# Performance work log

Hardware: AMD Instinct MI355X
Metric: run time of the kernel (lower is better)

## Reference

```python
import jax, jax.numpy as jnp
import numpy as np

ENC = 1024
DEC = 1024


def setup_inputs() -> dict:
    key = jax.random.key(0)
    k = jax.random.split(key, 8)
    s1 = 1.0 / np.sqrt(ENC)
    s2 = 1.0 / np.sqrt(DEC)
    return {
        "encoder_outputs": jax.random.normal(k[0], (32, 2048, ENC), jnp.float32),
        "decoder_output": jax.random.normal(k[1], (32, 1, DEC), jnp.float32),
        "w1": jax.random.uniform(k[2], (ENC, ENC), jnp.float32, -s1, s1),
        "b1": jax.random.uniform(k[3], (ENC,), jnp.float32, -s1, s1),
        "w2": jax.random.uniform(k[4], (DEC, ENC), jnp.float32, -s2, s2),
        "b2": jax.random.uniform(k[5], (ENC,), jnp.float32, -s2, s2),
        "v": jax.random.uniform(k[6], (ENC, 1), jnp.float32, -s1, s1),
        "bv": jax.random.uniform(k[7], (1,), jnp.float32, -s1, s1),
    }


def reference(encoder_outputs, decoder_output, w1, b1, w2, b2, v, bv):
    # [B,1,E] query projection, broadcast-added to [B,S,E] key projection
    w2_dec = jnp.einsum("bqd,de->bqe", decoder_output, w2) + b2
    w1_enc = jnp.einsum("bsd,de->bse", encoder_outputs, w1) + b1
    scores = jnp.einsum("bse,eo->bso", jnp.tanh(w1_enc + w2_dec), v) + bv  # [B,S,1]
    attn = jax.nn.softmax(scores[..., 0], axis=1)  # softmax over sequence dim
    context = jnp.einsum("bs,bse->be", attn, encoder_outputs)  # [B,E]
    return context
```

## Files before the change

kernel.cpp:

```cpp
#include <hip/hip_runtime.h>
#include <hip/hip_bf16.h>


typedef __attribute__((ext_vector_type(8))) short short8;
typedef __attribute__((ext_vector_type(4))) float f32x4;

#define M_TOTAL 65536
#define KDIM    1024

static __device__ inline unsigned int pk2h(float a, float b) {
    unsigned int ua = __builtin_bit_cast(unsigned int, a) + 0x8000u;
    unsigned int ub = __builtin_bit_cast(unsigned int, b) + 0x8000u;
    return __builtin_amdgcn_perm(ub, ua, 0x07060302u);
}

static __device__ inline void async_copy16(const void* g, void* l) {
    __builtin_amdgcn_global_load_lds(
        (const __attribute__((address_space(1))) unsigned int*)g,
        (__attribute__((address_space(3))) unsigned int*)l, 16, 0, 0);
}

__global__ void pack_w1(const float* __restrict__ w1, unsigned short* __restrict__ w1p) {
    __shared__ float tile[32][33];
    const int tx = threadIdx.x, ty = threadIdx.y;
    tile[ty][tx] = w1[(blockIdx.y * 32 + ty) * 1024 + blockIdx.x * 32 + tx];
    __syncthreads();
    const int eo = blockIdx.x * 32 + ty;
    const int dq = blockIdx.y * 32 + tx;
    const unsigned int u = __builtin_bit_cast(unsigned int, tile[tx][ty]) + 0x8000u;
    const unsigned short us = (unsigned short)(u >> 16);
    const int nt = eo >> 7, r = eo & 127;
    const int kc = dq >> 6, c = (dq >> 3) & 7, j = dq & 7;
    const int cs = c ^ (r & 7);
    w1p[(((size_t)(nt * 16 + kc)) << 13) + (r << 6) + (cs << 3) + j] = us;
}

__global__ __launch_bounds__(256) void qq_kern(const float* __restrict__ dec,
                                               const float* __restrict__ w2,
                                               const float* __restrict__ b1,
                                               const float* __restrict__ b2,
                                               float* __restrict__ qq) {
    const int b = blockIdx.y;
    const int e = blockIdx.x * 256 + threadIdx.x;
    const int d0 = blockIdx.z * 256;
    const float* db = dec + b * 1024;
    float acc = (blockIdx.z == 0) ? (b1[e] + b2[e]) : 0.f;
#pragma unroll 8
    for (int d = d0; d < d0 + 256; d++)
        acc = fmaf(db[d], w2[d * 1024 + e], acc);
    atomicAdd(&qq[b * 1024 + e], acc);
}

static __device__ inline void score_epilogue(f32x4 acc[4][4], const float* qqb,
                                             const float* vvec, float* scores,
                                             int m0, int n0, int wm, int wn,
                                             int quad, int lc) {
    const int nb = n0 + wn * 64 + lc;
    float qn[4], vn[4];
#pragma unroll
    for (int ni = 0; ni < 4; ni++) {
        qn[ni] = qqb[nb + ni * 16];
        vn[ni] = vvec[nb + ni * 16];
    }
    float red[16];
#pragma unroll
    for (int mi = 0; mi < 4; mi++) {
#pragma unroll
        for (int r = 0; r < 4; r++) {
            float ssum = 0.f;
#pragma unroll
            for (int ni = 0; ni < 4; ni++) {
                float x = acc[mi][ni][r] + qn[ni];
                float e = __expf(2.0f * x);
                float th = 1.0f - 2.0f / (e + 1.0f);
                ssum = fmaf(th, vn[ni], ssum);
            }
            float t = ssum;
            t += __shfl_xor(t, 1);
            t += __shfl_xor(t, 2);
            t += __shfl_xor(t, 4);
            t += __shfl_xor(t, 8);
            red[mi * 4 + r] = t;
        }
    }
    float myv = red[0];
#pragma unroll
    for (int i = 1; i < 16; i++)
        if (lc == i) myv = red[i];
    atomicAdd(scores + m0 + wm * 64 + (lc >> 2) * 16 + quad * 4 + (lc & 3), myv);
}

__global__ __launch_bounds__(256) void score_gemm(const float* __restrict__ enc,
                                                  const unsigned short* __restrict__ w1p,
                                                  const float* __restrict__ qq,
                                                  const float* __restrict__ vvec,
                                                  float* __restrict__ scores) {
    __shared__ __align__(16) unsigned short As[128 * 64];
    __shared__ __align__(16) unsigned short Bs[128 * 64];

    const int g = blockIdx.x;
    const int mtile = (g & 7) * 64 + (g >> 6);
    const int ntile = (g >> 3) & 7;
    const int m0 = mtile * 128;
    const int b = m0 >> 11;

    const int tid = threadIdx.x;
    const int wid = tid >> 6;
    const int lane = tid & 63;
    const int wm = wid >> 1, wn = wid & 1;
    const int quad = lane >> 4, lc = lane & 15;
    const int swz = lc & 7;
    const int fc0 = ((quad ^ swz) << 3);
    const int fc1 = (((4 + quad) ^ swz) << 3);

    const int sr0 = tid >> 3;
    const int sc = tid & 7;

    f32x4 acc[4][4];
#pragma unroll
    for (int mi = 0; mi < 4; mi++)
#pragma unroll
        for (int ni = 0; ni < 4; ni++)
            acc[mi][ni] = (f32x4){0.f, 0.f, 0.f, 0.f};

    const unsigned short* bbase = w1p + ((size_t)ntile << 17) + (wid << 11) + (lane << 3);
    unsigned short* bdst = &Bs[wid << 11];

    for (int k0 = 0; k0 < KDIM; k0 += 64) {
        __syncthreads();

        const unsigned short* bsrc = bbase + (((size_t)(k0 >> 6)) << 13);
        async_copy16(bsrc, bdst);
        async_copy16(bsrc + 512, bdst + 512);
        async_copy16(bsrc + 1024, bdst + 1024);
        async_copy16(bsrc + 1536, bdst + 1536);

        float4 fv[8];
#pragma unroll
        for (int j = 0; j < 4; j++) {
            const float* src = enc + (size_t)(m0 + sr0 + 32 * j) * 1024 + k0 + sc * 8;
            fv[2 * j]     = *reinterpret_cast<const float4*>(src);
            fv[2 * j + 1] = *reinterpret_cast<const float4*>(src + 4);
        }
#pragma unroll
        for (int j = 0; j < 4; j++) {
            const int r = sr0 + 32 * j;
            uint4 w;
            w.x = pk2h(fv[2 * j].x, fv[2 * j].y);
            w.y = pk2h(fv[2 * j].z, fv[2 * j].w);
            w.z = pk2h(fv[2 * j + 1].x, fv[2 * j + 1].y);
            w.w = pk2h(fv[2 * j + 1].z, fv[2 * j + 1].w);
            *reinterpret_cast<uint4*>(&As[(r << 6) + ((sc ^ (r & 7)) << 3)]) = w;
        }

        __syncthreads();

        short8 af[4], bf[4];
#pragma unroll
        for (int i = 0; i < 4; i++) {
            af[i] = *reinterpret_cast<const short8*>(&As[((wm * 64 + i * 16 + lc) << 6) + fc0]);
            bf[i] = *reinterpret_cast<const short8*>(&Bs[((wn * 64 + i * 16 + lc) << 6) + fc0]);
        }
#pragma unroll
        for (int mi = 0; mi < 4; mi++)
#pragma unroll
            for (int ni = 0; ni < 4; ni++)
                acc[mi][ni] = __builtin_amdgcn_mfma_f32_16x16x32_bf16(af[mi], bf[ni], acc[mi][ni], 0, 0, 0);
#pragma unroll
        for (int i = 0; i < 4; i++) {
            af[i] = *reinterpret_cast<const short8*>(&As[((wm * 64 + i * 16 + lc) << 6) + fc1]);
            bf[i] = *reinterpret_cast<const short8*>(&Bs[((wn * 64 + i * 16 + lc) << 6) + fc1]);
        }
#pragma unroll
        for (int mi = 0; mi < 4; mi++)
#pragma unroll
            for (int ni = 0; ni < 4; ni++)
                acc[mi][ni] = __builtin_amdgcn_mfma_f32_16x16x32_bf16(af[mi], bf[ni], acc[mi][ni], 0, 0, 0);
    }

    score_epilogue(acc, qq + b * 1024, vvec, scores, m0, ntile * 128, wm, wn, quad, lc);
}

__global__ __launch_bounds__(256) void softmax_kern(const float* __restrict__ scores,
                                                    float* __restrict__ attn) {
    const int b = blockIdx.x;
    const int tid = threadIdx.x;
    const int wid = tid >> 6, lane = tid & 63;
    const float* s = scores + b * 2048;
    float x[8];
    float m = -1e30f;
#pragma unroll
    for (int i = 0; i < 8; i++) {
        x[i] = s[tid + i * 256];
        m = fmaxf(m, x[i]);
    }
    for (int off = 1; off < 64; off <<= 1) m = fmaxf(m, __shfl_xor(m, off));
    __shared__ float redm[4];
    if (lane == 0) redm[wid] = m;
    __syncthreads();
    m = fmaxf(fmaxf(redm[0], redm[1]), fmaxf(redm[2], redm[3]));
    float sum = 0.f;
#pragma unroll
    for (int i = 0; i < 8; i++) {
        x[i] = __expf(x[i] - m);
        sum += x[i];
    }
    for (int off = 1; off < 64; off <<= 1) sum += __shfl_xor(sum, off);
    __shared__ float reds[4];
    if (lane == 0) reds[wid] = sum;
    __syncthreads();
    sum = reds[0] + reds[1] + reds[2] + reds[3];
    const float inv = 1.0f / sum;
#pragma unroll
    for (int i = 0; i < 8; i++) attn[b * 2048 + tid + i * 256] = x[i] * inv;
}

__global__ __launch_bounds__(256) void ctx_kern(const float* __restrict__ attn,
                                                const float* __restrict__ enc,
                                                float* __restrict__ out) {
    const int b = blockIdx.y;
    const int sc = blockIdx.x;
    const int tid = threadIdx.x;
    const float* ab = attn + b * 2048 + sc * 64;
    const float* eb = enc + ((size_t)b * 2048 + sc * 64) * 1024 + tid * 4;
    float4 acc = {0.f, 0.f, 0.f, 0.f};
#pragma unroll 16
    for (int s = 0; s < 64; s++) {
        float w = ab[s];
        float4 ev = *reinterpret_cast<const float4*>(eb + (size_t)s * 1024);
        acc.x = fmaf(w, ev.x, acc.x);
        acc.y = fmaf(w, ev.y, acc.y);
        acc.z = fmaf(w, ev.z, acc.z);
        acc.w = fmaf(w, ev.w, acc.w);
    }
    float* op = out + b * 1024 + tid * 4;
    atomicAdd(op + 0, acc.x);
    atomicAdd(op + 1, acc.y);
    atomicAdd(op + 2, acc.z);
    atomicAdd(op + 3, acc.w);
}

extern "C" void kernel_launch(void* const* d_in, const int* in_sizes, int n_in,
                              void* d_out, int out_size, void* d_ws, size_t ws_size,
                              hipStream_t stream) {
    const float* enc = (const float*)d_in[0];
    const float* dec = (const float*)d_in[1];
    const float* w1  = (const float*)d_in[2];
    const float* b1  = (const float*)d_in[3];
    const float* w2  = (const float*)d_in[4];
    const float* b2  = (const float*)d_in[5];
    const float* v   = (const float*)d_in[6];
    float* out = (float*)d_out;

    char* ws = (char*)d_ws;
    unsigned short* w1p = (unsigned short*)ws;
    float* qq     = (float*)(ws + (2u << 20));
    float* scores = (float*)(ws + (2u << 20) + (128u << 10));
    float* attn   = scores + M_TOTAL;

    hipMemsetAsync(qq, 0, (128u << 10) + M_TOTAL * sizeof(float), stream);
    hipMemsetAsync(out, 0, 32 * 1024 * sizeof(float), stream);

    pack_w1<<<dim3(32, 32), dim3(32, 32), 0, stream>>>(w1, w1p);
    qq_kern<<<dim3(4, 32, 4), 256, 0, stream>>>(dec, w2, b1, b2, qq);
    score_gemm<<<4096, 256, 0, stream>>>(enc, w1p, qq, v, scores);
    softmax_kern<<<32, 256, 0, stream>>>(scores, attn);
    ctx_kern<<<dim3(32, 32), 256, 0, stream>>>(attn, enc, out);
}
```

Measured before the change: 651.7 us.

## Double-buffer LDS tiles in score GEMM to overlap loads with MFMA

Turns the single-buffered K loop of the score GEMM into a two-stage software pipeline with ping-pong LDS buffers. The next tile's W1 async copy and encoder fp32 loads are issued before the current tile's MFMAs, and the bf16 pack into LDS happens after them, so global latency is meant to overlap compute. It also drops one barrier per iteration. LDS use doubles to 64KB per block and register pressure rises from holding the prefetched fv across compute, which can lower occupancy.

Measured after the change: 672.4 us. 1.03x slower.

```diff
diff --git a/kernel.cpp b/kernel.cpp
--- a/kernel.cpp
+++ b/kernel.cpp
@@ -7,6 +7,7 @@
 
 #define M_TOTAL 65536
 #define KDIM    1024
+#define KT_N    16
 
 static __device__ inline unsigned int pk2h(float a, float b) {
     unsigned int ua = __builtin_bit_cast(unsigned int, a) + 0x8000u;
@@ -95,8 +96,8 @@
                                                   const float* __restrict__ qq,
                                                   const float* __restrict__ vvec,
                                                   float* __restrict__ scores) {
-    __shared__ __align__(16) unsigned short As[128 * 64];
-    __shared__ __align__(16) unsigned short Bs[128 * 64];
+    __shared__ __align__(16) unsigned short As[2][128 * 64];
+    __shared__ __align__(16) unsigned short Bs[2][128 * 64];
 
     const int g = blockIdx.x;
     const int mtile = (g & 7) * 64 + (g >> 6);
@@ -124,24 +125,25 @@
             acc[mi][ni] = (f32x4){0.f, 0.f, 0.f, 0.f};
 
     const unsigned short* bbase = w1p + ((size_t)ntile << 17) + (wid << 11) + (lane << 3);
-    unsigned short* bdst = &Bs[wid << 11];
-
-    for (int k0 = 0; k0 < KDIM; k0 += 64) {
-        __syncthreads();
-
-        const unsigned short* bsrc = bbase + (((size_t)(k0 >> 6)) << 13);
+    float4 fv[8];
+
+    auto issueB = [&](int kt, int pb) {
+        const unsigned short* bsrc = bbase + ((size_t)kt << 13);
+        unsigned short* bdst = &Bs[pb][wid << 11];
         async_copy16(bsrc, bdst);
         async_copy16(bsrc + 512, bdst + 512);
         async_copy16(bsrc + 1024, bdst + 1024);
         async_copy16(bsrc + 1536, bdst + 1536);
-
-        float4 fv[8];
+    };
+    auto loadA = [&](int kt) {
 #pragma unroll
         for (int j = 0; j < 4; j++) {
-            const float* src = enc + (size_t)(m0 + sr0 + 32 * j) * 1024 + k0 + sc * 8;
+            const float* src = enc + (size_t)(m0 + sr0 + 32 * j) * 1024 + kt * 64 + sc * 8;
             fv[2 * j]     = *reinterpret_cast<const float4*>(src);
             fv[2 * j + 1] = *reinterpret_cast<const float4*>(src + 4);
         }
+    };
+    auto commitA = [&](int pb) {
 #pragma unroll
         for (int j = 0; j < 4; j++) {
             const int r = sr0 + 32 * j;
@@ -150,16 +152,15 @@
             w.y = pk2h(fv[2 * j].z, fv[2 * j].w);
             w.z = pk2h(fv[2 * j + 1].x, fv[2 * j + 1].y);
             w.w = pk2h(fv[2 * j + 1].z, fv[2 * j + 1].w);
-            *reinterpret_cast<uint4*>(&As[(r << 6) + ((sc ^ (r & 7)) << 3)]) = w;
-        }
-
-        __syncthreads();
-
+            *reinterpret_cast<uint4*>(&As[pb][(r << 6) + ((sc ^ (r & 7)) << 3)]) = w;
+        }
+    };
+    auto compute = [&](int pb) {
         short8 af[4], bf[4];
 #pragma unroll
         for (int i = 0; i < 4; i++) {
-            af[i] = *reinterpret_cast<const short8*>(&As[((wm * 64 + i * 16 + lc) << 6) + fc0]);
-            bf[i] = *reinterpret_cast<const short8*>(&Bs[((wn * 64 + i * 16 + lc) << 6) + fc0]);
+            af[i] = *reinterpret_cast<const short8*>(&As[pb][((wm * 64 + i * 16 + lc) << 6) + fc0]);
+            bf[i] = *reinterpret_cast<const short8*>(&Bs[pb][((wn * 64 + i * 16 + lc) << 6) + fc0]);
         }
 #pragma unroll
         for (int mi = 0; mi < 4; mi++)
@@ -168,14 +169,32 @@
                 acc[mi][ni] = __builtin_amdgcn_mfma_f32_16x16x32_bf16(af[mi], bf[ni], acc[mi][ni], 0, 0, 0);
 #pragma unroll
         for (int i = 0; i < 4; i++) {
-            af[i] = *reinterpret_cast<const short8*>(&As[((wm * 64 + i * 16 + lc) << 6) + fc1]);
-            bf[i] = *reinterpret_cast<const short8*>(&Bs[((wn * 64 + i * 16 + lc) << 6) + fc1]);
+            af[i] = *reinterpret_cast<const short8*>(&As[pb][((wm * 64 + i * 16 + lc) << 6) + fc1]);
+            bf[i] = *reinterpret_cast<const short8*>(&Bs[pb][((wn * 64 + i * 16 + lc) << 6) + fc1]);
         }
 #pragma unroll
         for (int mi = 0; mi < 4; mi++)
 #pragma unroll
             for (int ni = 0; ni < 4; ni++)
                 acc[mi][ni] = __builtin_amdgcn_mfma_f32_16x16x32_bf16(af[mi], bf[ni], acc[mi][ni], 0, 0, 0);
+    };
+
+    issueB(0, 0);
+    loadA(0);
+    commitA(0);
+    __syncthreads();
+
+#pragma unroll 2
+    for (int kt = 0; kt < KT_N; kt++) {
+        const int p = kt & 1;
+        if (kt + 1 < KT_N) {
+            issueB(kt + 1, p ^ 1);
+            loadA(kt + 1);
+        }
+        compute(p);
+        if (kt + 1 < KT_N)
+            commitA(p ^ 1);
+        __syncthreads();
     }
 
     score_epilogue(acc, qq + b * 1024, vvec, scores, m0, ntile * 128, wm, wn, quad, lc);
```

## Widen score GEMM N-tile to 256 and fuse prep and softmax-context kernels

Applied to the files above, without the earlier changes.

Merges the W1 packing, the query projection and the score zeroing into one prep kernel, replacing the memsets and separate launches. The score GEMM now uses 512-thread blocks with 256-wide N tiles, so each encoder A tile is loaded and converted to bf16 half as many times. Softmax is fused into the context kernel, with each block recomputing the softmax for its batch in LDS and reducing in shared memory instead of using atomics. This trades fewer launches and less redundant encoder traffic for larger blocks, more LDS and softmax work repeated across the 8 column blocks.

Result: slower. 683.2 us (+4.8%).

```diff
diff --git a/kernel.cpp b/kernel.cpp
--- a/kernel.cpp
+++ b/kernel.cpp
@@ -7,6 +7,7 @@
 
 #define M_TOTAL 65536
 #define KDIM    1024
+#define KT_N    16
 
 static __device__ inline unsigned int pk2h(float a, float b) {
     unsigned int ua = __builtin_bit_cast(unsigned int, a) + 0x8000u;
@@ -20,101 +21,87 @@
         (__attribute__((address_space(3))) unsigned int*)l, 16, 0, 0);
 }
 
-__global__ void pack_w1(const float* __restrict__ w1, unsigned short* __restrict__ w1p) {
-    __shared__ float tile[32][33];
-    const int tx = threadIdx.x, ty = threadIdx.y;
-    tile[ty][tx] = w1[(blockIdx.y * 32 + ty) * 1024 + blockIdx.x * 32 + tx];
-    __syncthreads();
-    const int eo = blockIdx.x * 32 + ty;
-    const int dq = blockIdx.y * 32 + tx;
-    const unsigned int u = __builtin_bit_cast(unsigned int, tile[tx][ty]) + 0x8000u;
-    const unsigned short us = (unsigned short)(u >> 16);
-    const int nt = eo >> 7, r = eo & 127;
-    const int kc = dq >> 6, c = (dq >> 3) & 7, j = dq & 7;
-    const int cs = c ^ (r & 7);
-    w1p[(((size_t)(nt * 16 + kc)) << 13) + (r << 6) + (cs << 3) + j] = us;
-}
-
-__global__ __launch_bounds__(256) void qq_kern(const float* __restrict__ dec,
-                                               const float* __restrict__ w2,
-                                               const float* __restrict__ b1,
-                                               const float* __restrict__ b2,
-                                               float* __restrict__ qq) {
-    const int b = blockIdx.y;
-    const int e = blockIdx.x * 256 + threadIdx.x;
-    const int d0 = blockIdx.z * 256;
-    const float* db = dec + b * 1024;
-    float acc = (blockIdx.z == 0) ? (b1[e] + b2[e]) : 0.f;
-#pragma unroll 8
-    for (int d = d0; d < d0 + 256; d++)
-        acc = fmaf(db[d], w2[d * 1024 + e], acc);
-    atomicAdd(&qq[b * 1024 + e], acc);
-}
-
-static __device__ inline void score_epilogue(f32x4 acc[4][4], const float* qqb,
-                                             const float* vvec, float* scores,
-                                             int m0, int n0, int wm, int wn,
-                                             int quad, int lc) {
-    const int nb = n0 + wn * 64 + lc;
-    float qn[4], vn[4];
-#pragma unroll
-    for (int ni = 0; ni < 4; ni++) {
-        qn[ni] = qqb[nb + ni * 16];
-        vn[ni] = vvec[nb + ni * 16];
-    }
-    float red[16];
-#pragma unroll
-    for (int mi = 0; mi < 4; mi++) {
-#pragma unroll
-        for (int r = 0; r < 4; r++) {
-            float ssum = 0.f;
-#pragma unroll
-            for (int ni = 0; ni < 4; ni++) {
-                float x = acc[mi][ni][r] + qn[ni];
-                float e = __expf(2.0f * x);
-                float th = 1.0f - 2.0f / (e + 1.0f);
-                ssum = fmaf(th, vn[ni], ssum);
-            }
-            float t = ssum;
-            t += __shfl_xor(t, 1);
-            t += __shfl_xor(t, 2);
-            t += __shfl_xor(t, 4);
-            t += __shfl_xor(t, 8);
-            red[mi * 4 + r] = t;
-        }
-    }
-    float myv = red[0];
-#pragma unroll
-    for (int i = 1; i < 16; i++)
-        if (lc == i) myv = red[i];
-    atomicAdd(scores + m0 + wm * 64 + (lc >> 2) * 16 + quad * 4 + (lc & 3), myv);
-}
-
-__global__ __launch_bounds__(256) void score_gemm(const float* __restrict__ enc,
+__global__ __launch_bounds__(256) void prep(const float* __restrict__ w1,
+                                            unsigned short* __restrict__ w1p,
+                                            const float* __restrict__ dec,
+                                            const float* __restrict__ w2,
+                                            const float* __restrict__ b1,
+                                            const float* __restrict__ b2,
+                                            float* __restrict__ qq,
+                                            float* __restrict__ scores) {
+    const int blk = blockIdx.x;
+    const int t = threadIdx.x;
+    if (blk < 1024) {
+        __shared__ float tile[32][33];
+        const int bx = blk & 31, by = blk >> 5;
+        const int col = t & 31, rq = t >> 5;
+#pragma unroll
+        for (int q = 0; q < 4; q++) {
+            const int row = rq * 4 + q;
+            tile[row][col] = w1[(by * 32 + row) * 1024 + bx * 32 + col];
+        }
+        __syncthreads();
+#pragma unroll
+        for (int q = 0; q < 4; q++) {
+            const int ty = rq * 4 + q;
+            const int eo = bx * 32 + ty;
+            const int dq = by * 32 + col;
+            const unsigned int u = __builtin_bit_cast(unsigned int, tile[col][ty]) + 0x8000u;
+            const unsigned short us = (unsigned short)(u >> 16);
+            const int nt = eo >> 8, r = eo & 255;
+            const int kc = dq >> 6, c = (dq >> 3) & 7, j = dq & 7;
+            const int cs = c ^ (r & 7);
+            w1p[(((size_t)(nt * 16 + kc)) << 14) + (r << 6) + (cs << 3) + j] = us;
+        }
+    } else if (blk < 1056) {
+        const int ec = blk - 1024;
+        const int e = ec * 32 + (t & 31);
+        const int b0 = t >> 5;
+        float acc[4] = {0.f, 0.f, 0.f, 0.f};
+#pragma unroll 4
+        for (int d = 0; d < 1024; d++) {
+            const float w2v = w2[d * 1024 + e];
+#pragma unroll
+            for (int i = 0; i < 4; i++)
+                acc[i] = fmaf(dec[(b0 + 8 * i) * 1024 + d], w2v, acc[i]);
+        }
+        const float bias = b1[e] + b2[e];
+#pragma unroll
+        for (int i = 0; i < 4; i++)
+            qq[(b0 + 8 * i) * 1024 + e] = acc[i] + bias;
+    } else {
+        const int z = blk - 1056;
+        const float4 zero = {0.f, 0.f, 0.f, 0.f};
+        *reinterpret_cast<float4*>(scores + z * 1024 + t * 4) = zero;
+    }
+}
+
+__global__ __launch_bounds__(512) void score_gemm(const float* __restrict__ enc,
                                                   const unsigned short* __restrict__ w1p,
                                                   const float* __restrict__ qq,
                                                   const float* __restrict__ vvec,
                                                   float* __restrict__ scores) {
     __shared__ __align__(16) unsigned short As[128 * 64];
-    __shared__ __align__(16) unsigned short Bs[128 * 64];
+    __shared__ __align__(16) unsigned short Bs[256 * 64];
 
     const int g = blockIdx.x;
-    const int mtile = (g & 7) * 64 + (g >> 6);
-    const int ntile = (g >> 3) & 7;
+    const int mtile = (g >> 5) * 8 + (g & 7);
+    const int ntile = (g >> 3) & 3;
     const int m0 = mtile * 128;
     const int b = m0 >> 11;
 
     const int tid = threadIdx.x;
     const int wid = tid >> 6;
     const int lane = tid & 63;
-    const int wm = wid >> 1, wn = wid & 1;
+    const int wm = wid >> 2, wn = wid & 3;
     const int quad = lane >> 4, lc = lane & 15;
     const int swz = lc & 7;
     const int fc0 = ((quad ^ swz) << 3);
     const int fc1 = (((4 + quad) ^ swz) << 3);
 
-    const int sr0 = tid >> 3;
-    const int sc = tid & 7;
+    const int r = tid >> 2, u = tid & 3;
+    const int aw0_off = (r << 6) + (((2 * u) ^ (r & 7)) << 3);
+    const int aw1_off = (r << 6) + (((2 * u + 1) ^ (r & 7)) << 3);
 
     f32x4 acc[4][4];
 #pragma unroll
@@ -123,35 +110,31 @@
         for (int ni = 0; ni < 4; ni++)
             acc[mi][ni] = (f32x4){0.f, 0.f, 0.f, 0.f};
 
-    const unsigned short* bbase = w1p + ((size_t)ntile << 17) + (wid << 11) + (lane << 3);
+    const unsigned short* bbase = w1p + ((size_t)ntile << 18) + (wid << 11) + (lane << 3);
     unsigned short* bdst = &Bs[wid << 11];
-
-    for (int k0 = 0; k0 < KDIM; k0 += 64) {
+    const float* abase = enc + (size_t)(m0 + r) * 1024 + u * 16;
+
+    for (int kt = 0; kt < KT_N; kt++) {
         __syncthreads();
 
-        const unsigned short* bsrc = bbase + (((size_t)(k0 >> 6)) << 13);
+        const unsigned short* bsrc = bbase + ((size_t)kt << 14);
         async_copy16(bsrc, bdst);
         async_copy16(bsrc + 512, bdst + 512);
         async_copy16(bsrc + 1024, bdst + 1024);
         async_copy16(bsrc + 1536, bdst + 1536);
 
-        float4 fv[8];
-#pragma unroll
-        for (int j = 0; j < 4; j++) {
-            const float* src = enc + (size_t)(m0 + sr0 + 32 * j) * 1024 + k0 + sc * 8;
-            fv[2 * j]     = *reinterpret_cast<const float4*>(src);
-            fv[2 * j + 1] = *reinterpret_cast<const float4*>(src + 4);
-        }
-#pragma unroll
-        for (int j = 0; j < 4; j++) {
-            const int r = sr0 + 32 * j;
-            uint4 w;
-            w.x = pk2h(fv[2 * j].x, fv[2 * j].y);
-            w.y = pk2h(fv[2 * j].z, fv[2 * j].w);
-            w.z = pk2h(fv[2 * j + 1].x, fv[2 * j + 1].y);
-            w.w = pk2h(fv[2 * j + 1].z, fv[2 * j + 1].w);
-            *reinterpret_cast<uint4*>(&As[(r << 6) + ((sc ^ (r & 7)) << 3)]) = w;
-        }
+        const float* asrc = abase + kt * 64;
+        const float4 f0 = *reinterpret_cast<const float4*>(asrc);
+        const float4 f1 = *reinterpret_cast<const float4*>(asrc + 4);
+        const float4 f2 = *reinterpret_cast<const float4*>(asrc + 8);
+        const float4 f3 = *reinterpret_cast<const float4*>(asrc + 12);
+        uint4 w0, w1v;
+        w0.x = pk2h(f0.x, f0.y); w0.y = pk2h(f0.z, f0.w);
+        w0.z = pk2h(f1.x, f1.y); w0.w = pk2h(f1.z, f1.w);
+        w1v.x = pk2h(f2.x, f2.y); w1v.y = pk2h(f2.z, f2.w);
+        w1v.z = pk2h(f3.x, f3.y); w1v.w = pk2h(f3.z, f3.w);
+        *reinterpret_cast<uint4*>(&As[aw0_off]) = w0;
+        *reinterpret_cast<uint4*>(&As[aw1_off]) = w1v;
 
         __syncthreads();
 
@@ -178,24 +161,61 @@
                 acc[mi][ni] = __builtin_amdgcn_mfma_f32_16x16x32_bf16(af[mi], bf[ni], acc[mi][ni], 0, 0, 0);
     }
 
-    score_epilogue(acc, qq + b * 1024, vvec, scores, m0, ntile * 128, wm, wn, quad, lc);
-}
-
-__global__ __launch_bounds__(256) void softmax_kern(const float* __restrict__ scores,
-                                                    float* __restrict__ attn) {
-    const int b = blockIdx.x;
-    const int tid = threadIdx.x;
-    const int wid = tid >> 6, lane = tid & 63;
+    const float* qqb = qq + b * 1024;
+    const int nb = ntile * 256 + wn * 64 + lc;
+    float qn[4], vn[4];
+#pragma unroll
+    for (int ni = 0; ni < 4; ni++) {
+        qn[ni] = qqb[nb + ni * 16];
+        vn[ni] = vvec[nb + ni * 16];
+    }
+    float red[16];
+#pragma unroll
+    for (int mi = 0; mi < 4; mi++) {
+#pragma unroll
+        for (int rr = 0; rr < 4; rr++) {
+            float ssum = 0.f;
+#pragma unroll
+            for (int ni = 0; ni < 4; ni++) {
+                float x = acc[mi][ni][rr] + qn[ni];
+                float e = __expf(2.0f * x);
+                float th = 1.0f - 2.0f / (e + 1.0f);
+                ssum = fmaf(th, vn[ni], ssum);
+            }
+            float tt = ssum;
+            tt += __shfl_xor(tt, 1);
+            tt += __shfl_xor(tt, 2);
+            tt += __shfl_xor(tt, 4);
+            tt += __shfl_xor(tt, 8);
+            red[mi * 4 + rr] = tt;
+        }
+    }
+    float myv = red[0];
+#pragma unroll
+    for (int i = 1; i < 16; i++)
+        if (lc == i) myv = red[i];
+    atomicAdd(scores + m0 + wm * 64 + (lc >> 2) * 16 + quad * 4 + (lc & 3), myv);
+}
+
+__global__ __launch_bounds__(256) void ctx_softmax(const float* __restrict__ scores,
+                                                   const float* __restrict__ enc,
+                                                   float* __restrict__ out) {
+    const int ec = blockIdx.x, b = blockIdx.y;
+    const int t = threadIdx.x;
+    const int lane = t & 63, wid = t >> 6;
+    __shared__ float attn[2048];
+    __shared__ float redm[4], reds[4];
+    __shared__ float4 redc[8][32];
+
     const float* s = scores + b * 2048;
     float x[8];
     float m = -1e30f;
 #pragma unroll
     for (int i = 0; i < 8; i++) {
-        x[i] = s[tid + i * 256];
+        x[i] = s[t + i * 256];
         m = fmaxf(m, x[i]);
     }
-    for (int off = 1; off < 64; off <<= 1) m = fmaxf(m, __shfl_xor(m, off));
-    __shared__ float redm[4];
+    for (int o = 1; o < 64; o <<= 1) m = fmaxf(m, __shfl_xor(m, o));
     if (lane == 0) redm[wid] = m;
     __syncthreads();
     m = fmaxf(fmaxf(redm[0], redm[1]), fmaxf(redm[2], redm[3]));
@@ -205,39 +225,39 @@
         x[i] = __expf(x[i] - m);
         sum += x[i];
     }
-    for (int off = 1; off < 64; off <<= 1) sum += __shfl_xor(sum, off);
-    __shared__ float reds[4];
+    for (int o = 1; o < 64; o <<= 1) sum += __shfl_xor(sum, o);
     if (lane == 0) reds[wid] = sum;
     __syncthreads();
-    sum = reds[0] + reds[1] + reds[2] + reds[3];
-    const float inv = 1.0f / sum;
-#pragma unroll
-    for (int i = 0; i < 8; i++) attn[b * 2048 + tid + i * 256] = x[i] * inv;
-}
-
-__global__ __launch_bounds__(256) void ctx_kern(const float* __restrict__ attn,
-                                                const float* __restrict__ enc,
-                                                float* __restrict__ out) {
-    const int b = blockIdx.y;
-    const int sc = blockIdx.x;
-    const int tid = threadIdx.x;
-    const float* ab = attn + b * 2048 + sc * 64;
-    const float* eb = enc + ((size_t)b * 2048 + sc * 64) * 1024 + tid * 4;
+    const float inv = 1.0f / (reds[0] + reds[1] + reds[2] + reds[3]);
+#pragma unroll
+    for (int i = 0; i < 8; i++) attn[t + i * 256] = x[i] * inv;
+    __syncthreads();
+
+    const int e0 = ec * 128 + (t & 31) * 4;
+    const int sl = t >> 5;
+    const float* eb = enc + ((size_t)b * 2048 + sl * 256) * 1024 + e0;
+    const float* aw = attn + sl * 256;
     float4 acc = {0.f, 0.f, 0.f, 0.f};
-#pragma unroll 16
-    for (int s = 0; s < 64; s++) {
-        float w = ab[s];
-        float4 ev = *reinterpret_cast<const float4*>(eb + (size_t)s * 1024);
+#pragma unroll 8
+    for (int si = 0; si < 256; si++) {
+        const float w = aw[si];
+        const float4 ev = *reinterpret_cast<const float4*>(eb + (size_t)si * 1024);
         acc.x = fmaf(w, ev.x, acc.x);
         acc.y = fmaf(w, ev.y, acc.y);
         acc.z = fmaf(w, ev.z, acc.z);
         acc.w = fmaf(w, ev.w, acc.w);
     }
-    float* op = out + b * 1024 + tid * 4;
-    atomicAdd(op + 0, acc.x);
-    atomicAdd(op + 1, acc.y);
-    atomicAdd(op + 2, acc.z);
-    atomicAdd(op + 3, acc.w);
+    redc[sl][t & 31] = acc;
+    __syncthreads();
+    if (t < 32) {
+        float4 a = redc[0][t];
+#pragma unroll
+        for (int i = 1; i < 8; i++) {
+            const float4 v = redc[i][t];
+            a.x += v.x; a.y += v.y; a.z += v.z; a.w += v.w;
+        }
+        *reinterpret_cast<float4*>(out + b * 1024 + ec * 128 + t * 4) = a;
+    }
 }
 
 extern "C" void kernel_launch(void* const* d_in, const int* in_sizes, int n_in,
@@ -256,14 +276,8 @@
     unsigned short* w1p = (unsigned short*)ws;
     float* qq     = (float*)(ws + (2u << 20));
     float* scores = (float*)(ws + (2u << 20) + (128u << 10));
-    float* attn   = scores + M_TOTAL;
-
-    hipMemsetAsync(qq, 0, (128u << 10) + M_TOTAL * sizeof(float), stream);
-    hipMemsetAsync(out, 0, 32 * 1024 * sizeof(float), stream);
-
-    pack_w1<<<dim3(32, 32), dim3(32, 32), 0, stream>>>(w1, w1p);
-    qq_kern<<<dim3(4, 32, 4), 256, 0, stream>>>(dec, w2, b1, b2, qq);
-    score_gemm<<<4096, 256, 0, stream>>>(enc, w1p, qq, v, scores);
-    softmax_kern<<<32, 256, 0, stream>>>(scores, attn);
-    ctx_kern<<<dim3(32, 32), 256, 0, stream>>>(attn, enc, out);
-}
+
+    prep<<<1120, 256, 0, stream>>>(w1, w1p, dec, w2, b1, b2, qq, scores);
+    score_gemm<<<2048, 512, 0, stream>>>(enc, w1p, qq, v, scores);
+    ctx_softmax<<<dim3(8, 32), 256, 0, stream>>>(scores, enc, out);
+}
```
